# Performance work log

Measured on AMD Instinct MI355X. Metric: run time of the kernel, lower is better.

Reference implementation:

```python
import jax, jax.numpy as jnp
import numpy as np

N = 100000  # nodes
E = 1600000  # edges


def gcn_conv(x, W, b, src, dst, n_nodes):
    """PyG-style GCNConv: add self-loops, symmetric norm, linear, scatter-add, bias."""
    h = x @ W  # [N, F_out]
    loop = jnp.arange(n_nodes, dtype=src.dtype)
    s = jnp.concatenate([src, loop])  # source nodes (messages flow src -> dst)
    d = jnp.concatenate([dst, loop])
    deg = jax.ops.segment_sum(jnp.ones_like(d, dtype=h.dtype), d, num_segments=n_nodes)
    dinv = jnp.where(deg > 0, jax.lax.rsqrt(deg), 0.0)
    norm = dinv[s] * dinv[d]  # [E+N]
    msgs = h[s] * norm[:, None]  # [E+N, F_out] -- dominant memory traffic
    out = jax.ops.segment_sum(msgs, d, num_segments=n_nodes)
    return out + b


def setup_inputs() -> dict:
    key = jax.random.key(0)
    k1, k2, k3, k4 = jax.random.split(key, 4)
    x = jax.random.normal(k1, (N, 128), dtype=jnp.float32)
    edge_index = jax.random.randint(k2, (2, E), 0, N, dtype=jnp.int32)
    W1 = jax.random.normal(k3, (128, 64), dtype=jnp.float32) * (1.0 / np.sqrt(128))
    b1 = jnp.zeros((64,), dtype=jnp.float32)
    W2 = jax.random.normal(k4, (64, 16), dtype=jnp.float32) * (1.0 / np.sqrt(64))
    b2 = jnp.zeros((16,), dtype=jnp.float32)
    return {"x": x, "edge_index": edge_index, "W1": W1, "b1": b1, "W2": W2, "b2": b2}


def reference(x, edge_index, W1, b1, W2, b2):
    src, dst = edge_index[0], edge_index[1]
    h = gcn_conv(x, W1, b1, src, dst, N)
    h = jax.nn.leaky_relu(h, negative_slope=0.2)
    # dropout is identity in eval mode
    h = gcn_conv(h, W2, b2, src, dst, N)
    return jax.nn.log_softmax(h, axis=-1)
```

## Files before the change

kernel.cpp:

```cpp
#include <hip/hip_runtime.h>
#include <math.h>


#define CHUNK 4096
#define BSHIFT 9
#define BMASK 511
#define CAP 9216
#define CAPP (CAP + 40)

typedef __bf16 bf16x8 __attribute__((ext_vector_type(8)));
typedef float f32x4 __attribute__((ext_vector_type(4)));

__device__ __forceinline__ unsigned f2b(float f) {
  unsigned u = __float_as_uint(f);
  return (u + 0x7FFF + ((u >> 16) & 1)) >> 16;
}

struct f2 { float x, y; };
__device__ __forceinline__ void addu(f2& a, unsigned u) {
  a.x += __uint_as_float(u << 16);
  a.y += __uint_as_float(u);
}
__device__ __forceinline__ void addu4(f2* a, uint4 g) {
  addu(a[0], g.x); addu(a[1], g.y); addu(a[2], g.z); addu(a[3], g.w);
}

__global__ void binit_kernel(int* __restrict__ gbcursor, int nbc,
                             unsigned* __restrict__ h1s, unsigned* __restrict__ t,
                             int n) {
  int b = blockIdx.x * 256 + threadIdx.x;
  if (b < nbc) gbcursor[b] = b * CAP;
  if (blockIdx.x == 0) {
    if (threadIdx.x < 32) h1s[(size_t)n * 32 + threadIdx.x] = 0u;
    else if (threadIdx.x < 40) t[(size_t)n * 8 + (threadIdx.x - 32)] = 0u;
  }
}

__global__ __launch_bounds__(256) void scatterA_kernel(const int* __restrict__ src,
                                                       const int* __restrict__ dst,
                                                       int E, int nbc,
                                                       int* __restrict__ gbcursor,
                                                       int* __restrict__ tmp) {
  __shared__ int hist[256];
  __shared__ int segcur[256];
  int tid = threadIdx.x;
  int estart = blockIdx.x * CHUNK;
  int eend = min(E, estart + CHUNK);
  hist[tid] = 0;
  __syncthreads();
  for (int i = estart + tid; i < eend; i += 256)
    atomicAdd(&hist[dst[i] >> BSHIFT], 1);
  __syncthreads();
  if (tid < nbc) {
    int c = hist[tid];
    segcur[tid] = c ? atomicAdd(&gbcursor[tid], c) : 0;
  }
  __syncthreads();
  for (int i = estart + tid; i < eend; i += 256) {
    int d = dst[i];
    int b = d >> BSHIFT;
    int pos = atomicAdd(&segcur[b], 1);
    if (pos < (b + 1) * CAP)
      tmp[pos] = (src[i] << BSHIFT) | (d & BMASK);
  }
}

__global__ __launch_bounds__(512) void degcnt_kernel(const int* __restrict__ tmp,
                                                     const int* __restrict__ gbcursor,
                                                     float* __restrict__ dinv, int n) {
  __shared__ int nh[512];
  int b = blockIdx.x, tid = threadIdx.x;
  nh[tid] = 0;
  __syncthreads();
  int base = b * CAP;
  int count = min(gbcursor[b] - base, CAP);
  for (int i = tid; i < count; i += 512) atomicAdd(&nh[tmp[base + i] & BMASK], 1);
  __syncthreads();
  int v = (b << BSHIFT) + tid;
  if (v < n) dinv[v] = rsqrtf((float)(nh[tid] + 1));
}

__global__ __launch_bounds__(256, 4) void gemm1_kernel(const float* __restrict__ x,
                                                       const float* __restrict__ W1,
                                                       const float* __restrict__ dinv,
                                                       unsigned* __restrict__ h1s, int n) {
  __shared__ unsigned lds_u[64 * 68 * 2];
  unsigned* xs = lds_u;
  unsigned* wt = lds_u + 64 * 68;
  int tid = threadIdx.x;
  int vb = blockIdx.x * 64;
  int nrows = min(64, n - vb);

  const float4* xg = (const float4*)(x + (size_t)vb * 128);
#pragma unroll
  for (int it = 0; it < 8; ++it) {
    int idx = it * 256 + tid;
    int r = idx >> 5, c2 = idx & 31;
    float4 vv = make_float4(0.f, 0.f, 0.f, 0.f);
    if (r < nrows) vv = xg[idx];
    xs[r * 68 + c2 * 2] = (f2b(vv.y) << 16) | f2b(vv.x);
    xs[r * 68 + c2 * 2 + 1] = (f2b(vv.w) << 16) | f2b(vv.z);
  }
  unsigned short* wt16 = (unsigned short*)wt;
  const float4* wg = (const float4*)W1;
#pragma unroll
  for (int it = 0; it < 8; ++it) {
    int idx = it * 256 + tid;
    int k = idx >> 4, n0 = (idx & 15) * 4;
    float4 wv = wg[idx];
    wt16[(n0 + 0) * 136 + k] = (unsigned short)f2b(wv.x);
    wt16[(n0 + 1) * 136 + k] = (unsigned short)f2b(wv.y);
    wt16[(n0 + 2) * 136 + k] = (unsigned short)f2b(wv.z);
    wt16[(n0 + 3) * 136 + k] = (unsigned short)f2b(wv.w);
  }
  __syncthreads();

  int lane = tid & 63, wid = tid >> 6;
  int m16 = lane & 15, quad = lane >> 4;
  const unsigned* xp = xs + (wid * 16 + m16) * 68 + quad * 4;
  const unsigned* wp = wt + m16 * 68 + quad * 4;
  f32x4 acc[4] = {};
#pragma unroll
  for (int ks = 0; ks < 4; ++ks) {
    bf16x8 a = *(const bf16x8*)(xp + ks * 16);
#pragma unroll
    for (int nt = 0; nt < 4; ++nt) {
      bf16x8 b = *(const bf16x8*)(wp + nt * 16 * 68 + ks * 16);
      acc[nt] = __builtin_amdgcn_mfma_f32_16x16x32_bf16(a, b, acc[nt], 0, 0, 0);
    }
  }
  int rbase = vb + wid * 16 + quad * 4;
  float dvv[4];
#pragma unroll
  for (int reg = 0; reg < 4; ++reg) {
    int row = rbase + reg;
    dvv[reg] = (row < n) ? dinv[row] : 0.f;
  }
  unsigned short* h16 = (unsigned short*)h1s;
#pragma unroll
  for (int nt = 0; nt < 4; ++nt) {
    int col = nt * 16 + m16;
#pragma unroll
    for (int reg = 0; reg < 4; ++reg) {
      int row = rbase + reg;
      if (row < n)
        h16[(size_t)row * 64 + col] = (unsigned short)f2b(dvv[reg] * acc[nt][reg]);
    }
  }
}

template <int NQ>
__device__ __forceinline__ void gatherTier1(const uint4* __restrict__ h1s4,
                                            const int* lcsr, int rs, int e1,
                                            int e, int c, int n, f2* a0) {
  int cv0[NQ], cv1[NQ];
#pragma unroll
  for (int q = 0; q < NQ; ++q) {
    cv0[q] = lcsr[rs + q * 8 + e];
    cv1[q] = lcsr[rs + q * 8 + 4 + e];
  }
  uint4 g[2 * NQ];
#pragma unroll
  for (int q = 0; q < NQ; ++q) {
    int k0 = rs + q * 8 + e, k1 = k0 + 4;
    int s0 = (k0 < e1) ? cv0[q] : n;
    int s1 = (k1 < e1) ? cv1[q] : n;
    g[2 * q] = h1s4[(size_t)s0 * 8 + c];
    g[2 * q + 1] = h1s4[(size_t)s1 * 8 + c];
  }
#pragma unroll
  for (int k = 0; k < 2 * NQ; ++k) addu4(a0, g[k]);
}

__global__ __launch_bounds__(1024) void agg1_fused_kernel(
    const int* __restrict__ tmp, const int* __restrict__ gbcursor,
    const uint4* __restrict__ h1s4, const float* __restrict__ dinv,
    const float* __restrict__ b1, const float* __restrict__ W2,
    int* __restrict__ row_start, int* __restrict__ degs, int* __restrict__ csr,
    unsigned* __restrict__ t, int n) {
  __shared__ int lcsr[CAPP];
  __shared__ int nh[512];
  __shared__ int rs_s[512];
  __shared__ int lcur[512];
  __shared__ float W2s[64 * 17];
  __shared__ float b1s[64];
  __shared__ float a_s[16][2][64];
  int b = blockIdx.x, tid = threadIdx.x;
  int base = b * CAP;
  int count = min(gbcursor[b] - base, CAP);

  if (tid < 512) nh[tid] = 0;
  W2s[(tid >> 4) * 17 + (tid & 15)] = W2[tid];
  if (tid < 64) b1s[tid] = b1[tid];
  __syncthreads();
  for (int i = tid; i < count; i += 1024) atomicAdd(&nh[tmp[base + i] & BMASK], 1);
  __syncthreads();
  int d = 0;
  if (tid < 512) { d = nh[tid]; rs_s[tid] = d; }
  __syncthreads();
  for (int off = 1; off < 512; off <<= 1) {
    int a = 0;
    if (tid < 512) { a = rs_s[tid]; if (tid >= off) a += rs_s[tid - off]; }
    __syncthreads();
    if (tid < 512) rs_s[tid] = a;
    __syncthreads();
  }
  if (tid < 512) {
    int e0 = rs_s[tid] - d;
    lcur[tid] = e0;
    rs_s[tid] = e0;
    int v = (b << BSHIFT) + tid;
    if (v < n) { row_start[v] = base + e0; degs[v] = d; }
  }
  __syncthreads();
  for (int i = tid; i < count; i += 1024) {
    int val = tmp[base + i];
    int pos = atomicAdd(&lcur[val & BMASK], 1);
    lcsr[pos] = val >> BSHIFT;
  }
  __syncthreads();
  for (int i = tid; i < count; i += 1024) csr[base + i] = lcsr[i];

  int wave = tid >> 6, lane = tid & 63;
  int half = lane >> 5, sub = lane & 31;
  int e = sub >> 3, c = sub & 7;
  int j = sub & 15, grp = (sub >> 4) & 1;

#pragma unroll 1
  for (int it = 0; it < 16; ++it) {
    int nl = wave * 32 + it * 2 + half;
    int v = (b << BSHIFT) + nl;
    bool valid = (v < n);
    int rs = rs_s[nl];
    int deg = nh[nl];
    int e1 = rs + deg;
    float dv = valid ? dinv[valid ? v : 0] : 0.f;

    f2 a0[4];
#pragma unroll
    for (int k = 0; k < 4; ++k) a0[k] = {0.f, 0.f};
    {
      int s = (valid && sub < 8) ? v : n;
      addu4(a0, h1s4[(size_t)s * 8 + c]);
    }
    int dm = max(deg, __shfl_xor(deg, 32, 64));
    int start;
    if (dm <= 16) {
      gatherTier1<2>(h1s4, lcsr, rs, e1, e, c, n, a0);
      start = 16;
    } else if (dm <= 24) {
      gatherTier1<3>(h1s4, lcsr, rs, e1, e, c, n, a0);
      start = 24;
    } else {
      gatherTier1<4>(h1s4, lcsr, rs, e1, e, c, n, a0);
      start = 32;
    }
    int i = rs + start;
    while (__any(i < e1)) {
      int i0 = i + e, i1 = i + 4 + e;
      int s0v = lcsr[i0];
      int s1v = lcsr[i1];
      int s0 = (i0 < e1) ? s0v : n;
      int s1 = (i1 < e1) ? s1v : n;
      addu4(a0, h1s4[(size_t)s0 * 8 + c]);
      addu4(a0, h1s4[(size_t)s1 * 8 + c]);
      i += 8;
    }
#pragma unroll
    for (int m = 8; m <= 16; m <<= 1) {
#pragma unroll
      for (int k = 0; k < 4; ++k) {
        a0[k].x += __shfl_xor(a0[k].x, m, 64);
        a0[k].y += __shfl_xor(a0[k].y, m, 64);
      }
    }
    if (sub < 8) {
#pragma unroll
      for (int k = 0; k < 4; ++k) {
        float z0 = fmaf(dv, a0[k].x, b1s[8 * sub + 2 * k]);
        float z1 = fmaf(dv, a0[k].y, b1s[8 * sub + 2 * k + 1]);
        a_s[wave][half][8 * sub + 2 * k] = fmaxf(z0, 0.2f * z0);
        a_s[wave][half][8 * sub + 2 * k + 1] = fmaxf(z1, 0.2f * z1);
      }
    }
    float p = 0.f;
#pragma unroll
    for (int q = 0; q < 16; ++q) {
      int f = grp * 16 + q;
      p = fmaf(a_s[wave][half][f], W2s[f * 17 + j], p);
    }
#pragma unroll
    for (int q = 0; q < 16; ++q) {
      int f = 32 + grp * 16 + q;
      p = fmaf(a_s[wave][half][f], W2s[f * 17 + j], p);
    }
    p += __shfl_xor(p, 16, 64);
    float pv = dv * p;
    float po = __shfl_xor(pv, 1, 64);
    if (valid && sub < 16 && !(sub & 1))
      t[(size_t)v * 8 + (sub >> 1)] = (f2b(po) << 16) | f2b(pv);
  }
}

template <int NQ>
__device__ __forceinline__ void gatherTier2(const uint4* __restrict__ t4,
                                            const int* __restrict__ csr, int rs,
                                            int e1, int e, int c, int n, f2* A0) {
  int cv[NQ];
#pragma unroll
  for (int q = 0; q < NQ; ++q) cv[q] = csr[rs + q * 8 + e];
  uint4 g[NQ];
#pragma unroll
  for (int q = 0; q < NQ; ++q) {
    int k = rs + q * 8 + e;
    int s = (k < e1) ? cv[q] : n;
    g[q] = t4[(size_t)s * 2 + c];
  }
#pragma unroll
  for (int k = 0; k < NQ; ++k) addu4(A0, g[k]);
}

__global__ __launch_bounds__(256) void agg2_kernel(const uint4* __restrict__ t4,
                                                   const float* __restrict__ dinv,
                                                   const int* __restrict__ row_start,
                                                   const int* __restrict__ degs,
                                                   const int* __restrict__ csr,
                                                   const float* __restrict__ b2,
                                                   float* __restrict__ out, int n) {
  int idx = blockIdx.x * 256 + threadIdx.x;
  int v = idx >> 4;
  if (v >= n) return;
  int sub = threadIdx.x & 15;
  int e = sub >> 1, c = sub & 1;
  float dv = dinv[v];
  int rs = row_start[v], deg = degs[v], e1 = rs + deg;
  f2 A0[4];
#pragma unroll
  for (int k = 0; k < 4; ++k) A0[k] = {0.f, 0.f};
  {
    int s = (e == 0) ? v : n;
    addu4(A0, t4[(size_t)s * 2 + c]);
  }
  int m1 = max(deg, __shfl_xor(deg, 16, 64));
  int dm = max(m1, __shfl_xor(m1, 32, 64));
  int start;
  if (dm <= 16) {
    gatherTier2<2>(t4, csr, rs, e1, e, c, n, A0);
    start = 16;
  } else if (dm <= 24) {
    gatherTier2<3>(t4, csr, rs, e1, e, c, n, A0);
    start = 24;
  } else {
    gatherTier2<4>(t4, csr, rs, e1, e, c, n, A0);
    start = 32;
  }
  int i = rs + start;
  while (__any(i < e1)) {
    int i0 = i + e;
    int sv = csr[i0];
    int s = (i0 < e1) ? sv : n;
    addu4(A0, t4[(size_t)s * 2 + c]);
    i += 8;
  }
#pragma unroll
  for (int m = 2; m <= 8; m <<= 1) {
#pragma unroll
    for (int k = 0; k < 4; ++k) {
      A0[k].x += __shfl_xor(A0[k].x, m, 64);
      A0[k].y += __shfl_xor(A0[k].y, m, 64);
    }
  }
  float4 bb0 = ((const float4*)b2)[c * 2];
  float4 bb1 = ((const float4*)b2)[c * 2 + 1];
  float z[8];
  z[0] = fmaf(dv, A0[0].x, bb0.x); z[1] = fmaf(dv, A0[0].y, bb0.y);
  z[2] = fmaf(dv, A0[1].x, bb0.z); z[3] = fmaf(dv, A0[1].y, bb0.w);
  z[4] = fmaf(dv, A0[2].x, bb1.x); z[5] = fmaf(dv, A0[2].y, bb1.y);
  z[6] = fmaf(dv, A0[3].x, bb1.z); z[7] = fmaf(dv, A0[3].y, bb1.w);
  float mx = z[0];
#pragma unroll
  for (int q = 1; q < 8; ++q) mx = fmaxf(mx, z[q]);
  mx = fmaxf(mx, __shfl_xor(mx, 1, 64));
  float ss = 0.f;
#pragma unroll
  for (int q = 0; q < 8; ++q) ss += expf(z[q] - mx);
  ss += __shfl_xor(ss, 1, 64);
  float lg = mx + logf(ss);
  if (e == 0) {
    float4 r0 = make_float4(z[0] - lg, z[1] - lg, z[2] - lg, z[3] - lg);
    float4 r1 = make_float4(z[4] - lg, z[5] - lg, z[6] - lg, z[7] - lg);
    float4* o = (float4*)out + (size_t)v * 4 + c * 2;
    o[0] = r0;
    o[1] = r1;
  }
}

extern "C" void kernel_launch(void* const* d_in, const int* in_sizes, int n_in,
                              void* d_out, int out_size, void* d_ws, size_t ws_size,
                              hipStream_t stream) {
  const float* x = (const float*)d_in[0];
  const int* edge_index = (const int*)d_in[1];
  const float* W1 = (const float*)d_in[2];
  const float* b1 = (const float*)d_in[3];
  const float* W2 = (const float*)d_in[4];
  const float* b2 = (const float*)d_in[5];
  float* out = (float*)d_out;

  int N_ = in_sizes[0] / 128;
  int E_ = in_sizes[1] / 2;
  const int* src = edge_index;
  const int* dst = edge_index + E_;
  int NBc = (N_ + BMASK) >> BSHIFT;

  char* ws = (char*)d_ws;
  size_t off = 0;
  auto take = [&](size_t bytes) {
    void* p = ws + off;
    off += (bytes + 255) & ~(size_t)255;
    return p;
  };
  unsigned* h1s = (unsigned*)take(((size_t)N_ + 1) * 32 * 4);
  unsigned* t = (unsigned*)take(((size_t)N_ + 1) * 8 * 4);
  int* tmp = (int*)take((size_t)NBc * CAP * 4);
  int* csr = (int*)take(((size_t)NBc * CAP + 64) * 4);
  float* dinv = (float*)take((size_t)N_ * 4);
  int* degs = (int*)take((size_t)N_ * 4);
  int* row_start = (int*)take((size_t)N_ * 4);
  int* gbcursor = (int*)take((size_t)NBc * 4);
  (void)ws_size;

  binit_kernel<<<(NBc + 255) / 256, 256, 0, stream>>>(gbcursor, NBc, h1s, t, N_);
  scatterA_kernel<<<(E_ + CHUNK - 1) / CHUNK, 256, 0, stream>>>(src, dst, E_, NBc,
                                                                gbcursor, tmp);
  degcnt_kernel<<<NBc, 512, 0, stream>>>(tmp, gbcursor, dinv, N_);
  gemm1_kernel<<<(N_ + 63) / 64, 256, 0, stream>>>(x, W1, dinv, h1s, N_);
  agg1_fused_kernel<<<NBc, 1024, 0, stream>>>(tmp, gbcursor, (const uint4*)h1s,
                                              dinv, b1, W2, row_start, degs, csr,
                                              t, N_);
  agg2_kernel<<<(N_ * 16 + 255) / 256, 256, 0, stream>>>((const uint4*)t, dinv,
                                                         row_start, degs, csr,
                                                         b2, out, N_);
}
```

Before: 202.2 us.

## Halve dst bucket size, reuse degree counts, simplify agg2 gather

```diff
diff --git a/kernel.cpp b/kernel.cpp
--- a/kernel.cpp
+++ b/kernel.cpp
@@ -3,9 +3,9 @@
 
 
 #define CHUNK 4096
-#define BSHIFT 9
-#define BMASK 511
-#define CAP 9216
+#define BSHIFT 8
+#define BMASK 255
+#define CAP 4864
 #define CAPP (CAP + 40)
 
 typedef __bf16 bf16x8 __attribute__((ext_vector_type(8)));
@@ -41,19 +41,20 @@
                                                        int E, int nbc,
                                                        int* __restrict__ gbcursor,
                                                        int* __restrict__ tmp) {
-  __shared__ int hist[256];
-  __shared__ int segcur[256];
+  __shared__ int hist[512];
+  __shared__ int segcur[512];
   int tid = threadIdx.x;
   int estart = blockIdx.x * CHUNK;
   int eend = min(E, estart + CHUNK);
   hist[tid] = 0;
+  hist[tid + 256] = 0;
   __syncthreads();
   for (int i = estart + tid; i < eend; i += 256)
     atomicAdd(&hist[dst[i] >> BSHIFT], 1);
   __syncthreads();
-  if (tid < nbc) {
-    int c = hist[tid];
-    segcur[tid] = c ? atomicAdd(&gbcursor[tid], c) : 0;
+  for (int bb = tid; bb < nbc; bb += 256) {
+    int c = hist[bb];
+    segcur[bb] = c ? atomicAdd(&gbcursor[bb], c) : 0;
   }
   __syncthreads();
   for (int i = estart + tid; i < eend; i += 256) {
@@ -65,19 +66,23 @@
   }
 }
 
-__global__ __launch_bounds__(512) void degcnt_kernel(const int* __restrict__ tmp,
+__global__ __launch_bounds__(256) void degcnt_kernel(const int* __restrict__ tmp,
                                                      const int* __restrict__ gbcursor,
+                                                     int* __restrict__ degs,
                                                      float* __restrict__ dinv, int n) {
-  __shared__ int nh[512];
+  __shared__ int nh[256];
   int b = blockIdx.x, tid = threadIdx.x;
   nh[tid] = 0;
   __syncthreads();
   int base = b * CAP;
   int count = min(gbcursor[b] - base, CAP);
-  for (int i = tid; i < count; i += 512) atomicAdd(&nh[tmp[base + i] & BMASK], 1);
+  for (int i = tid; i < count; i += 256) atomicAdd(&nh[tmp[base + i] & BMASK], 1);
   __syncthreads();
   int v = (b << BSHIFT) + tid;
-  if (v < n) dinv[v] = rsqrtf((float)(nh[tid] + 1));
+  if (v < n) {
+    degs[v] = nh[tid];
+    dinv[v] = rsqrtf((float)(nh[tid] + 1));
+  }
 }
 
 __global__ __launch_bounds__(256, 4) void gemm1_kernel(const float* __restrict__ x,
@@ -176,12 +181,12 @@
     const int* __restrict__ tmp, const int* __restrict__ gbcursor,
     const uint4* __restrict__ h1s4, const float* __restrict__ dinv,
     const float* __restrict__ b1, const float* __restrict__ W2,
-    int* __restrict__ row_start, int* __restrict__ degs, int* __restrict__ csr,
-    unsigned* __restrict__ t, int n) {
+    const int* __restrict__ degs, int* __restrict__ row_start,
+    int* __restrict__ csr, unsigned* __restrict__ t, int n) {
   __shared__ int lcsr[CAPP];
-  __shared__ int nh[512];
-  __shared__ int rs_s[512];
-  __shared__ int lcur[512];
+  __shared__ int nh[256];
+  __shared__ int rs_s[256];
+  __shared__ int lcur[256];
   __shared__ float W2s[64 * 17];
   __shared__ float b1s[64];
   __shared__ float a_s[16][2][64];
@@ -189,28 +194,28 @@
   int base = b * CAP;
   int count = min(gbcursor[b] - base, CAP);
 
-  if (tid < 512) nh[tid] = 0;
+  if (tid < 256) {
+    int v = (b << BSHIFT) + tid;
+    int d = (v < n) ? degs[v] : 0;
+    nh[tid] = d;
+    rs_s[tid] = d;
+  }
   W2s[(tid >> 4) * 17 + (tid & 15)] = W2[tid];
   if (tid < 64) b1s[tid] = b1[tid];
   __syncthreads();
-  for (int i = tid; i < count; i += 1024) atomicAdd(&nh[tmp[base + i] & BMASK], 1);
-  __syncthreads();
-  int d = 0;
-  if (tid < 512) { d = nh[tid]; rs_s[tid] = d; }
-  __syncthreads();
-  for (int off = 1; off < 512; off <<= 1) {
+  for (int off = 1; off < 256; off <<= 1) {
     int a = 0;
-    if (tid < 512) { a = rs_s[tid]; if (tid >= off) a += rs_s[tid - off]; }
+    if (tid < 256) { a = rs_s[tid]; if (tid >= off) a += rs_s[tid - off]; }
     __syncthreads();
-    if (tid < 512) rs_s[tid] = a;
+    if (tid < 256) rs_s[tid] = a;
     __syncthreads();
   }
-  if (tid < 512) {
-    int e0 = rs_s[tid] - d;
+  if (tid < 256) {
+    int e0 = rs_s[tid] - nh[tid];
     lcur[tid] = e0;
     rs_s[tid] = e0;
     int v = (b << BSHIFT) + tid;
-    if (v < n) { row_start[v] = base + e0; degs[v] = d; }
+    if (v < n) row_start[v] = base + e0;
   }
   __syncthreads();
   for (int i = tid; i < count; i += 1024) {
@@ -227,8 +232,8 @@
   int j = sub & 15, grp = (sub >> 4) & 1;
 
 #pragma unroll 1
-  for (int it = 0; it < 16; ++it) {
-    int nl = wave * 32 + it * 2 + half;
+  for (int it = 0; it < 8; ++it) {
+    int nl = wave * 16 + it * 2 + half;
     int v = (b << BSHIFT) + nl;
     bool valid = (v < n);
     int rs = rs_s[nl];
@@ -300,24 +305,6 @@
     if (valid && sub < 16 && !(sub & 1))
       t[(size_t)v * 8 + (sub >> 1)] = (f2b(po) << 16) | f2b(pv);
   }
-}
-
-template <int NQ>
-__device__ __forceinline__ void gatherTier2(const uint4* __restrict__ t4,
-                                            const int* __restrict__ csr, int rs,
-                                            int e1, int e, int c, int n, f2* A0) {
-  int cv[NQ];
-#pragma unroll
-  for (int q = 0; q < NQ; ++q) cv[q] = csr[rs + q * 8 + e];
-  uint4 g[NQ];
-#pragma unroll
-  for (int q = 0; q < NQ; ++q) {
-    int k = rs + q * 8 + e;
-    int s = (k < e1) ? cv[q] : n;
-    g[q] = t4[(size_t)s * 2 + c];
-  }
-#pragma unroll
-  for (int k = 0; k < NQ; ++k) addu4(A0, g[k]);
 }
 
 __global__ __launch_bounds__(256) void agg2_kernel(const uint4* __restrict__ t4,
@@ -333,7 +320,7 @@
   int sub = threadIdx.x & 15;
   int e = sub >> 1, c = sub & 1;
   float dv = dinv[v];
-  int rs = row_start[v], deg = degs[v], e1 = rs + deg;
+  int rs = row_start[v], e1 = rs + degs[v];
   f2 A0[4];
 #pragma unroll
   for (int k = 0; k < 4; ++k) A0[k] = {0.f, 0.f};
@@ -341,21 +328,20 @@
     int s = (e == 0) ? v : n;
     addu4(A0, t4[(size_t)s * 2 + c]);
   }
-  int m1 = max(deg, __shfl_xor(deg, 16, 64));
-  int dm = max(m1, __shfl_xor(m1, 32, 64));
-  int start;
-  if (dm <= 16) {
-    gatherTier2<2>(t4, csr, rs, e1, e, c, n, A0);
-    start = 16;
-  } else if (dm <= 24) {
-    gatherTier2<3>(t4, csr, rs, e1, e, c, n, A0);
-    start = 24;
-  } else {
-    gatherTier2<4>(t4, csr, rs, e1, e, c, n, A0);
-    start = 32;
-  }
-  int i = rs + start;
-  while (__any(i < e1)) {
+  int cv[4];
+#pragma unroll
+  for (int q = 0; q < 4; ++q) cv[q] = csr[rs + q * 8 + e];
+  uint4 g[4];
+#pragma unroll
+  for (int q = 0; q < 4; ++q) {
+    int k = rs + q * 8 + e;
+    int s = (k < e1) ? cv[q] : n;
+    g[q] = t4[(size_t)s * 2 + c];
+  }
+#pragma unroll
+  for (int k = 0; k < 4; ++k) addu4(A0, g[k]);
+  int i = rs + 32;
+  while (i < e1) {
     int i0 = i + e;
     int sv = csr[i0];
     int s = (i0 < e1) ? sv : n;
@@ -432,10 +418,10 @@
   binit_kernel<<<(NBc + 255) / 256, 256, 0, stream>>>(gbcursor, NBc, h1s, t, N_);
   scatterA_kernel<<<(E_ + CHUNK - 1) / CHUNK, 256, 0, stream>>>(src, dst, E_, NBc,
                                                                 gbcursor, tmp);
-  degcnt_kernel<<<NBc, 512, 0, stream>>>(tmp, gbcursor, dinv, N_);
+  degcnt_kernel<<<NBc, 256, 0, stream>>>(tmp, gbcursor, degs, dinv, N_);
   gemm1_kernel<<<(N_ + 63) / 64, 256, 0, stream>>>(x, W1, dinv, h1s, N_);
   agg1_fused_kernel<<<NBc, 1024, 0, stream>>>(tmp, gbcursor, (const uint4*)h1s,
-                                              dinv, b1, W2, row_start, degs, csr,
+                                              dinv, b1, W2, degs, row_start, csr,
                                               t, N_);
   agg2_kernel<<<(N_ * 16 + 255) / 256, 256, 0, stream>>>((const uint4*)t, dinv,
                                                          row_start, degs, csr,
```

Result: no change. 203.4 us (+0.6%).
